# Performance work log

Hardware: AMD Instinct MI355X
Metric: run time of the kernel (lower is better)

The kernel has to match this reference:

```python
import jax, jax.numpy as jnp
import numpy as np

L = 3          # num_layers
EPS = 1e-5     # BatchNorm eps


def _gmn_forward(feats_1, feats_2, edge_index_1, edge_index_2, N1, N2,
                 Wn, bn, Wm, bm, Wp, bp, gamma, beta, Wa, ba, Wg, bg, Wf, bf):
    N = N1 + N2
    x = jnp.concatenate([feats_1, feats_2], axis=0)                       # [N, F]
    edge_index = jnp.concatenate([edge_index_1, edge_index_2 + N1], axis=1)
    src, dst = edge_index[0], edge_index[1]                               # source_to_target flow
    batch = jnp.concatenate([jnp.zeros((N1,), jnp.int32), jnp.ones((N2,), jnp.int32)])
    for l in range(L):
        h = x @ Wn[l] + bn[l]                                             # lin_node
        # message(x_i=h[dst], x_j=h[src]) = lin_message(cat[x_i, x_j])
        m = jnp.concatenate([h[dst], h[src]], axis=1) @ Wm[l] + bm[l]     # [E, D]
        aggr = jax.ops.segment_sum(m, dst, num_segments=N)                # scatter-add to targets
        # batch_block_pair_attention on ORIGINAL (pre-lin_node) features
        gx, gy = x[:N1], x[N1:]
        s = gx @ gy.T                                                     # [N1, N2] similarities
        att_x = jax.nn.softmax(s, axis=1) @ gy                            # attn for graph-1 nodes
        att_y = jax.nn.softmax(s, axis=0).T @ gx                          # attn for graph-2 nodes
        cross = jnp.concatenate([att_x, att_y], axis=0)                   # [N, F]
        att_in = x - cross                                                # attention_input
        out = jnp.concatenate([aggr, att_in], axis=1) @ Wp[l] + bp[l]     # lin_passing
        mu = out.mean(axis=0)
        var = ((out - mu) ** 2).mean(axis=0)                              # BatchNorm (train, biased var)
        x = (out - mu) * jax.lax.rsqrt(var + EPS) * gamma[l] + beta[l]
    # GraphAggregator
    states = x @ Wa + ba
    gates = jax.nn.softmax(x @ Wg + bg, axis=1)                           # softmax over feature dim (as in source)
    g = states * gates
    sums = jax.ops.segment_sum(g, batch, num_segments=2)                  # scatter_mean
    counts = jnp.array([N1, N2], jnp.float32)[:, None]
    emb = (sums / counts) @ Wf + bf                                       # [2, D]
    return emb


def setup_inputs() -> dict:
    key = jax.random.key(0)
    ks = jax.random.split(key, 12)
    N1 = N2 = 6144
    E = 196608
    F = 128
    D = 128
    sc = lambda fan: fan ** -0.5
    rn = lambda k, sh, s: jax.random.normal(k, sh, dtype=jnp.float32) * s
    return {
        "feats_1": rn(ks[0], (N1, F), 1.0),
        "edge_index_1": jax.random.randint(ks[1], (2, E), 0, N1),
        "feats_2": rn(ks[2], (N2, F), 1.0),
        "edge_index_2": jax.random.randint(ks[3], (2, E), 0, N2),
        "sizes_1": N1,
        "sizes_2": N2,
        "Wn": rn(ks[4], (L, F, D), sc(F)),
        "bn": jnp.zeros((L, D), jnp.float32),
        "Wm": rn(ks[5], (L, 2 * D, D), sc(2 * D)),
        "bm": jnp.zeros((L, D), jnp.float32),
        "Wp": rn(ks[6], (L, D + F, D), sc(D + F)),
        "bp": jnp.zeros((L, D), jnp.float32),
        "gamma": jnp.ones((L, D), jnp.float32),
        "beta": jnp.zeros((L, D), jnp.float32),
        "Wa": rn(ks[7], (D, D), sc(D)),
        "ba": jnp.zeros((D,), jnp.float32),
        "Wg": rn(ks[8], (D, D), sc(D)),
        "bg": jnp.zeros((D,), jnp.float32),
        "Wf": rn(ks[9], (D, D), sc(D)),
        "bf": jnp.zeros((D,), jnp.float32),
    }


def reference(feats_1, edge_index_1, feats_2, edge_index_2, sizes_1, sizes_2,
              Wn, bn, Wm, bm, Wp, bp, gamma, beta, Wa, ba, Wg, bg, Wf, bf):
    emb = _gmn_forward(feats_1, feats_2, edge_index_1, edge_index_2,
                       int(sizes_1), int(sizes_2),
                       Wn, bn, Wm, bm, Wp, bp, gamma, beta, Wa, ba, Wg, bg, Wf, bf)
    emb_1 = emb[0:1]
    emb_2 = emb[1:2]
    return emb_1, emb_2
```

## Files before the change

### kernel.cpp

```cpp
#include <hip/hip_runtime.h>
#include <hip/hip_bf16.h>

#define D 128
#define KVS 8
typedef unsigned short u16;
typedef unsigned int u32;
typedef __attribute__((ext_vector_type(8))) short short8;
typedef __attribute__((ext_vector_type(16))) float f32x16;
typedef __attribute__((ext_vector_type(4))) u32 u32x4;

__device__ __forceinline__ u16 f2bf(float f){
  u32 u = __builtin_bit_cast(u32, f);
  u32 r = (u + 0x7FFFu + ((u >> 16) & 1u)) >> 16;
  return (u16)r;
}
__device__ __forceinline__ float bf2f(u16 u){
  union { u32 i; float f; } v; v.i = ((u32)u) << 16; return v.f;
}

__global__ void k_copy(const float* __restrict__ src, float* __restrict__ dst, int n4){
  int i = blockIdx.x*blockDim.x + threadIdx.x;
  for (; i < n4; i += gridDim.x*blockDim.x){
    ((float4*)dst)[i] = ((const float4*)src)[i];
  }
}

__global__ void k_count(const int* __restrict__ ei1, const int* __restrict__ ei2,
                        int E1, int E2, int N1, int* __restrict__ cnt){
  int i = blockIdx.x*blockDim.x + threadIdx.x;
  int Et = E1 + E2;
  for (; i < Et; i += gridDim.x*blockDim.x){
    int dst = (i < E1) ? ei1[E1 + i] : (ei2[E2 + (i - E1)] + N1);
    atomicAdd(&cnt[dst], 1);
  }
}

__global__ void k_scan(const int* __restrict__ cnt, int* __restrict__ ptr,
                       int* __restrict__ cursor, float* __restrict__ degf, int N){
  __shared__ int part[256];
  int t = threadIdx.x;
  int per = (N + 255) >> 8;
  int lo = t*per, hi = min(N, lo+per);
  int s = 0;
  for (int j=lo;j<hi;j++) s += cnt[j];
  part[t] = s; __syncthreads();
  if (t==0){ int acc=0; for (int j=0;j<256;j++){ int v=part[j]; part[j]=acc; acc+=v; } }
  __syncthreads();
  int acc = part[t];
  for (int j=lo;j<hi;j++){ ptr[j]=acc; cursor[j]=acc; degf[j]=(float)cnt[j]; acc += cnt[j]; }
}

__global__ void k_fill(const int* __restrict__ ei1, const int* __restrict__ ei2,
                       int E1, int E2, int N1, int* __restrict__ cursor, int* __restrict__ srclist){
  int i = blockIdx.x*blockDim.x + threadIdx.x;
  int Et = E1 + E2;
  for (; i < Et; i += gridDim.x*blockDim.x){
    int src, dst;
    if (i < E1){ src = ei1[i]; dst = ei1[E1+i]; }
    else { int j = i - E1; src = ei2[j] + N1; dst = ei2[E2+j] + N1; }
    int p = atomicAdd(&cursor[dst], 1);
    srclist[p] = src;
  }
}

__global__ __launch_bounds__(256) void k_wcvt(const float* __restrict__ Wn, const float* __restrict__ Wm,
                                              const float* __restrict__ Wp, u16* __restrict__ wgt){
  __shared__ u16 tile[128][136];
  int m = blockIdx.x;
  const float* src; u16* dst;
  if (m < 3){ src = Wn + m*16384; dst = wgt + m*16384; }
  else if (m < 9){ int l=(m-3)%3, half=(m-3)/3; src = Wm + l*32768 + half*16384; dst = wgt + (3 + half*3 + l)*16384; }
  else { int l=(m-9)%3, half=(m-9)/3; src = Wp + l*32768 + half*16384; dst = wgt + (9 + half*3 + l)*16384; }
  int t = threadIdx.x;
  int n = t & 127, rh = t >> 7;
  for (int r0=0; r0<128; r0+=2){
    int r = r0 + rh;
    tile[n][r] = f2bf(src[r*128 + n]);
  }
  __syncthreads();
  int row = t >> 1, ch = t & 1;
  #pragma unroll
  for (int i=0;i<4;i++){
    int k0 = ch*64 + i*16;
    short8 a = *(const short8*)&tile[row][k0];
    short8 b = *(const short8*)&tile[row][k0+8];
    *(short8*)&dst[row*128 + k0] = a;
    *(short8*)&dst[row*128 + k0 + 8] = b;
  }
}

__global__ __launch_bounds__(256) void k_cvt(const float* __restrict__ x, u16* __restrict__ xb,
                                             u16* __restrict__ xbT, int N){
  __shared__ u16 tile[128][136];
  int nb = blockIdx.x * 128;
  int t = threadIdx.x;
  int n = t >> 1;
  int ch = t & 1;
  #pragma unroll
  for (int i=0;i<16;i++){
    int dd = ch*64 + i*4;
    float4 v = *(const float4*)&x[(size_t)(nb+n)*D + dd];
    u16 b0 = f2bf(v.x), b1 = f2bf(v.y), b2 = f2bf(v.z), b3 = f2bf(v.w);
    ushort4 uv; uv.x=b0; uv.y=b1; uv.z=b2; uv.w=b3;
    *(ushort4*)&xb[(size_t)(nb+n)*D + dd] = uv;
    tile[dd+0][n]=b0; tile[dd+1][n]=b1; tile[dd+2][n]=b2; tile[dd+3][n]=b3;
  }
  __syncthreads();
  int d = t & 127, hf = t >> 7;
  #pragma unroll
  for (int i=0;i<8;i++){
    short8 v = *(const short8*)&tile[d][hf*64 + i*8];
    *(short8*)&xbT[(size_t)d*N + nb + hf*64 + i*8] = v;
  }
}

__global__ __launch_bounds__(256) void k_gemm(
    const u16* __restrict__ A, const u16* __restrict__ W1T,
    const u16* __restrict__ B, const u16* __restrict__ W2T,
    const float* __restrict__ bias, const float* __restrict__ rs,
    const float* __restrict__ addin,
    float* __restrict__ of, u16* __restrict__ ob, int N)
{
  __shared__ __align__(16) u16 Wsw[2][16384];
  const int t = threadIdx.x;
  const int w4 = t >> 6;
  const int lane = t & 63;
  const int l31 = lane & 31;
  const int hi = lane >> 5;
  const int rb = blockIdx.x * 32;

  #pragma unroll
  for (int i=0;i<8;i++){
    int slot = i*256 + t;
    int row = slot >> 4, g = slot & 15;
    short8 v = *(const short8*)(W1T + row*128 + g*8);
    *(short8*)((char*)&Wsw[0][0] + row*256 + ((g ^ (row&7))*16)) = v;
  }
  if (B){
    #pragma unroll
    for (int i=0;i<8;i++){
      int slot = i*256 + t;
      int row = slot >> 4, g = slot & 15;
      short8 v = *(const short8*)(W2T + row*128 + g*8);
      *(short8*)((char*)&Wsw[1][0] + row*256 + ((g ^ (row&7))*16)) = v;
    }
  }
  short8 af[8], bfr[8];
  #pragma unroll
  for (int g=0; g<8; g++)
    af[g] = *(const short8*)(A + (size_t)(rb + l31)*D + (2*g + hi)*8);
  if (B){
    #pragma unroll
    for (int g=0; g<8; g++)
      bfr[g] = *(const short8*)(B + (size_t)(rb + l31)*D + (2*g + hi)*8);
  }
  __syncthreads();

  f32x16 acc1, acc2;
  #pragma unroll
  for (int i=0;i<16;i++){ acc1[i]=0.f; acc2[i]=0.f; }
  const int wrow = w4*32 + l31;
  #pragma unroll
  for (int s=0;s<8;s++){
    int gr = 2*s + hi;
    short8 wf = *(const short8*)((const char*)&Wsw[0][0] + wrow*256 + ((gr ^ (wrow&7))*16));
    acc1 = __builtin_amdgcn_mfma_f32_32x32x16_bf16(af[s], wf, acc1, 0,0,0);
  }
  if (B){
    #pragma unroll
    for (int s=0;s<8;s++){
      int gr = 2*s + hi;
      short8 wf = *(const short8*)((const char*)&Wsw[1][0] + wrow*256 + ((gr ^ (wrow&7))*16));
      acc2 = __builtin_amdgcn_mfma_f32_32x32x16_bf16(bfr[s], wf, acc2, 0,0,0);
    }
  }
  const int col = wrow;
  float bv = bias ? bias[col] : 0.0f;
  #pragma unroll
  for (int r=0;r<16;r++){
    int rr = (r&3) + 8*(r>>2) + 4*hi;
    size_t grow = (size_t)(rb + rr);
    float v = acc1[r] + bv;
    if (rs) v *= rs[grow];
    if (B) v += acc2[r];
    if (addin) v += addin[grow*D + col];
    if (of) of[grow*D + col] = v;
    if (ob) ob[grow*D + col] = f2bf(v);
  }
}

__global__ __launch_bounds__(256) void k_gather(const u16* __restrict__ hb, const int* __restrict__ ptr,
                          const int* __restrict__ cnt, const int* __restrict__ srclist,
                          float* __restrict__ Sg, int N){
  int f = threadIdx.x & 127, sub = threadIdx.x >> 7;
  int v = blockIdx.x*2 + sub;
  if (v >= N) return;
  int b = ptr[v], n = cnt[v];
  float a0=0.f, a1=0.f, a2=0.f, a3=0.f;
  int j=0;
  for (; j+3<n; j+=4){
    int s0=srclist[b+j], s1=srclist[b+j+1], s2=srclist[b+j+2], s3=srclist[b+j+3];
    a0 += bf2f(hb[(size_t)s0*D + f]);
    a1 += bf2f(hb[(size_t)s1*D + f]);
    a2 += bf2f(hb[(size_t)s2*D + f]);
    a3 += bf2f(hb[(size_t)s3*D + f]);
  }
  for (; j<n; j++) a0 += bf2f(hb[(size_t)srclist[b+j]*D + f]);
  Sg[(size_t)v*D + f] = (a0+a1)+(a2+a3);
}

__global__ __launch_bounds__(256, 2) void k_flash_mfma(
    const u16* __restrict__ xb, const u16* __restrict__ xbT,
    int N1, int N2, int Ntot,
    float* __restrict__ Opart, float* __restrict__ MLpart)
{
  __shared__ __align__(16) u16 Kbuf[2][4096];
  __shared__ __align__(16) u16 Vbuf[2][4096];

  const int t = threadIdx.x;
  const int w = t >> 6;
  const int lane = t & 63;
  const int l31 = lane & 31;
  const int hi = lane >> 5;

  const int qb = blockIdx.x / KVS;
  const int sp = blockIdx.x % KVS;
  const int qbase = qb * 128;
  const int qs = qbase + w*32;
  const bool isY = qbase >= N1;
  const int kv0 = isY ? 0 : N1;
  const int kvlen = isY ? N1 : N2;
  const int Lk = kvlen / KVS;
  const int kstart = kv0 + sp*Lk;
  const int ntiles = Lk >> 5;

  short8 qf[8];
  #pragma unroll
  for (int c = 0; c < 8; ++c)
    qf[c] = *(const short8*)(xb + (size_t)(qs + l31)*D + c*16 + hi*8);

  const int kr = t >> 3;
  const int kg = (t & 7) * 2;
  const int vd = t >> 1;
  const int vj = (t & 1) * 2;
  const int kw0 = kr*256 + ((kg     ^ (kr & 7))*16);
  const int kw1 = kr*256 + (((kg+1) ^ (kr & 7))*16);
  const int vw0 = vd*64  + (((vj     ^ vd) & 3)*16);
  const int vw1 = vd*64  + ((((vj+1) ^ vd) & 3)*16);

  f32x16 O[4];
  #pragma unroll
  for (int mt=0; mt<4; ++mt)
    #pragma unroll
    for (int i=0;i<16;i++) O[mt][i] = 0.f;
  float m_run = -3.0e38f, l_run = 0.0f;

  {
    int kb = kstart;
    short8 a0 = *(const short8*)(xb  + (size_t)(kb+kr)*D + kg*8);
    short8 a1 = *(const short8*)(xb  + (size_t)(kb+kr)*D + (kg+1)*8);
    short8 v0 = *(const short8*)(xbT + (size_t)vd*Ntot + kb + vj*8);
    short8 v1 = *(const short8*)(xbT + (size_t)vd*Ntot + kb + (vj+1)*8);
    *(short8*)((char*)&Kbuf[0][0] + kw0) = a0;
    *(short8*)((char*)&Kbuf[0][0] + kw1) = a1;
    *(short8*)((char*)&Vbuf[0][0] + vw0) = v0;
    *(short8*)((char*)&Vbuf[0][0] + vw1) = v1;
  }
  __syncthreads();

  for (int tt = 0; tt < ntiles; ++tt){
    const int cur = tt & 1;
    const int nxt = cur ^ 1;
    short8 a0, a1, v0, v1;
    const bool more = (tt+1 < ntiles);
    if (more){
      int kb = kstart + (tt+1)*32;
      a0 = *(const short8*)(xb  + (size_t)(kb+kr)*D + kg*8);
      a1 = *(const short8*)(xb  + (size_t)(kb+kr)*D + (kg+1)*8);
      v0 = *(const short8*)(xbT + (size_t)vd*Ntot + kb + vj*8);
      v1 = *(const short8*)(xbT + (size_t)vd*Ntot + kb + (vj+1)*8);
    }

    const char* Klds = (const char*)&Kbuf[cur][0];
    const char* Vlds = (const char*)&Vbuf[cur][0];

    f32x16 sa, sb;
    #pragma unroll
    for (int i=0;i<16;i++){ sa[i]=0.f; sb[i]=0.f; }
    #pragma unroll
    for (int c = 0; c < 8; c += 2){
      int gr0 = 2*c + hi;
      short8 ka = *(const short8*)(Klds + l31*256 + ((gr0 ^ (l31&7))*16));
      sa = __builtin_amdgcn_mfma_f32_32x32x16_bf16(ka, qf[c], sa, 0,0,0);
      int gr1 = 2*(c+1) + hi;
      short8 kbf = *(const short8*)(Klds + l31*256 + ((gr1 ^ (l31&7))*16));
      sb = __builtin_amdgcn_mfma_f32_32x32x16_bf16(kbf, qf[c+1], sb, 0,0,0);
    }
    f32x16 s;
    #pragma unroll
    for (int i=0;i<16;i++) s[i] = sa[i] + sb[i];

    float tm = s[0];
    #pragma unroll
    for (int i=1;i<16;i++) tm = fmaxf(tm, s[i]);
    tm = fmaxf(tm, __shfl_xor(tm, 32, 64));
    if (__any(tm > m_run + 8.0f)){
      float mnew = fmaxf(m_run, tm);
      float alpha = __expf(m_run - mnew);
      l_run *= alpha;
      m_run = mnew;
      #pragma unroll
      for (int i=0;i<16;i++){ O[0][i]*=alpha; O[1][i]*=alpha; O[2][i]*=alpha; O[3][i]*=alpha; }
    }
    float rsum = 0.f;
    #pragma unroll
    for (int i=0;i<16;i++){ float p = __expf(s[i]-m_run); s[i]=p; rsum += p; }
    rsum += __shfl_xor(rsum, 32, 64);
    l_run += rsum;

    u32 pk[8];
    #pragma unroll
    for (int i=0;i<8;i++){
      u32 r;
      asm("v_cvt_pk_bf16_f32 %0, %1, %2" : "=v"(r) : "v"(s[2*i]), "v"(s[2*i+1]));
      pk[i] = r;
    }

    #pragma unroll
    for (int ks=0; ks<2; ++ks){
      u32 send0 = hi ? pk[(2*ks)*2+0] : pk[(2*ks+1)*2+0];
      u32 send1 = hi ? pk[(2*ks)*2+1] : pk[(2*ks+1)*2+1];
      u32 xv0 = (u32)__shfl_xor((int)send0, 32, 64);
      u32 xv1 = (u32)__shfl_xor((int)send1, 32, 64);
      u32 own0 = hi ? pk[(2*ks+1)*2+0] : pk[(2*ks)*2+0];
      u32 own1 = hi ? pk[(2*ks+1)*2+1] : pk[(2*ks)*2+1];
      u32x4 bv;
      bv.x = hi ? xv0 : own0;
      bv.y = hi ? xv1 : own1;
      bv.z = hi ? own0 : xv0;
      bv.w = hi ? own1 : xv1;
      short8 pf = __builtin_bit_cast(short8, bv);
      #pragma unroll
      for (int mt=0; mt<4; ++mt){
        int dd = mt*32 + l31;
        int j = 2*ks + hi;
        short8 vf = *(const short8*)(Vlds + dd*64 + (((j ^ dd) & 3)*16));
        O[mt] = __builtin_amdgcn_mfma_f32_32x32x16_bf16(vf, pf, O[mt], 0,0,0);
      }
    }

    if (more){
      *(short8*)((char*)&Kbuf[nxt][0] + kw0) = a0;
      *(short8*)((char*)&Kbuf[nxt][0] + kw1) = a1;
      *(short8*)((char*)&Vbuf[nxt][0] + vw0) = v0;
      *(short8*)((char*)&Vbuf[nxt][0] + vw1) = v1;
    }
    __syncthreads();
  }

  const int strip = qs >> 5;
  float* Od = Opart + ((size_t)strip*KVS + sp)*4096;
  #pragma unroll
  for (int mt=0; mt<4; ++mt){
    #pragma unroll
    for (int r=0;r<16;r++){
      int dd = mt*32 + (r&3) + 8*(r>>2) + 4*hi;
      Od[dd*32 + l31] = O[mt][r];
    }
  }
  if (lane < 32){
    float* mlp = MLpart + ((size_t)strip*KVS + sp)*64;
    mlp[l31*2+0] = m_run;
    mlp[l31*2+1] = l_run;
  }
}

__global__ __launch_bounds__(256) void k_fcomb(
    const float* __restrict__ Opart, const float* __restrict__ MLpart,
    const float* __restrict__ x, u16* __restrict__ attinb)
{
  __shared__ float cw[KVS][32];
  __shared__ float Tld[128][33];
  const int strip = blockIdx.x;
  const int t = threadIdx.x;
  if (t < 32){
    int q = t;
    const float* mlp = MLpart + (size_t)strip*KVS*64;
    float mv[KVS], lv[KVS];
    float M = -3.0e38f;
    #pragma unroll
    for (int s2=0;s2<KVS;s2++){ mv[s2]=mlp[s2*64+q*2]; lv[s2]=mlp[s2*64+q*2+1]; M = fmaxf(M, mv[s2]); }
    float L = 0.f;
    #pragma unroll
    for (int s2=0;s2<KVS;s2++){ float wv=__expf(mv[s2]-M); cw[s2][q]=wv; L += wv*lv[s2]; }
    float inv = 1.0f / L;
    #pragma unroll
    for (int s2=0;s2<KVS;s2++) cw[s2][q] *= inv;
  }
  __syncthreads();
  {
    const int d = t >> 1, q0 = (t & 1) * 16;
    const float* Ob = Opart + (size_t)strip*KVS*4096;
    float acc[16];
    #pragma unroll
    for (int j=0;j<16;j++) acc[j]=0.f;
    #pragma unroll
    for (int s2=0; s2<KVS; ++s2){
      const float* row = Ob + s2*4096 + d*32 + q0;
      #pragma unroll
      for (int j4=0;j4<16;j4+=4){
        float4 v = *(const float4*)&row[j4];
        acc[j4+0] += cw[s2][q0+j4+0]*v.x;
        acc[j4+1] += cw[s2][q0+j4+1]*v.y;
        acc[j4+2] += cw[s2][q0+j4+2]*v.z;
        acc[j4+3] += cw[s2][q0+j4+3]*v.w;
      }
    }
    #pragma unroll
    for (int j=0;j<16;j++) Tld[d][q0+j] = acc[j];
  }
  __syncthreads();
  {
    const int q = t >> 3, c0 = (t & 7) * 16;
    const size_t row = (size_t)(strip*32 + q)*D;
    #pragma unroll
    for (int i=0;i<16;i+=4){
      float4 xr = *(const float4*)&x[row + c0 + i];
      ushort4 o;
      o.x = f2bf(xr.x - Tld[c0+i+0][q]);
      o.y = f2bf(xr.y - Tld[c0+i+1][q]);
      o.z = f2bf(xr.z - Tld[c0+i+2][q]);
      o.w = f2bf(xr.w - Tld[c0+i+3][q]);
      *(ushort4*)&attinb[row + c0 + i] = o;
    }
  }
}

__global__ __launch_bounds__(256) void k_colsum(const float* __restrict__ outb, int N,
                                                float* __restrict__ sums){
  int f = threadIdx.x & 127, sub = threadIdx.x >> 7;
  float s=0.f, q=0.f;
  for (int r = blockIdx.x*2 + sub; r < N; r += gridDim.x*2){
    float v = outb[(size_t)r*D + f]; s += v; q += v*v;
  }
  atomicAdd(&sums[f], s);
  atomicAdd(&sums[128+f], q);
}

__global__ __launch_bounds__(256) void k_normcvt(const float* __restrict__ outb,
                        const float* __restrict__ sums,
                        const float* __restrict__ gamma, const float* __restrict__ beta,
                        int N, float* __restrict__ x, u16* __restrict__ xb, u16* __restrict__ xbT){
  __shared__ u16 tile[128][136];
  __shared__ float smu[128], srs[128], sg2[128], sb2[128];
  int t = threadIdx.x;
  if (t < 128){
    float mu = sums[t] / (float)N;
    float var = fmaxf(sums[128+t]/(float)N - mu*mu, 0.0f);
    smu[t]=mu; srs[t]=rsqrtf(var + 1e-5f);
    sg2[t]=gamma[t]; sb2[t]=beta[t];
  }
  __syncthreads();
  int nb = blockIdx.x * 128;
  int n = t >> 1, ch = t & 1;
  #pragma unroll
  for (int i=0;i<16;i++){
    int dd = ch*64 + i*4;
    float4 v = *(const float4*)&outb[(size_t)(nb+n)*D + dd];
    float4 y;
    y.x = (v.x - smu[dd+0])*srs[dd+0]*sg2[dd+0] + sb2[dd+0];
    y.y = (v.y - smu[dd+1])*srs[dd+1]*sg2[dd+1] + sb2[dd+1];
    y.z = (v.z - smu[dd+2])*srs[dd+2]*sg2[dd+2] + sb2[dd+2];
    y.w = (v.w - smu[dd+3])*srs[dd+3]*sg2[dd+3] + sb2[dd+3];
    *(float4*)&x[(size_t)(nb+n)*D + dd] = y;
    u16 b0=f2bf(y.x), b1=f2bf(y.y), b2=f2bf(y.z), b3=f2bf(y.w);
    ushort4 uv; uv.x=b0; uv.y=b1; uv.z=b2; uv.w=b3;
    *(ushort4*)&xb[(size_t)(nb+n)*D + dd] = uv;
    tile[dd+0][n]=b0; tile[dd+1][n]=b1; tile[dd+2][n]=b2; tile[dd+3][n]=b3;
  }
  __syncthreads();
  int d = t & 127, hf = t >> 7;
  #pragma unroll
  for (int i=0;i<8;i++){
    short8 v = *(const short8*)&tile[d][hf*64 + i*8];
    *(short8*)&xbT[(size_t)d*N + nb + hf*64 + i*8] = v;
  }
}

__global__ __launch_bounds__(256) void k_matmul(
    const float* __restrict__ A, const float* __restrict__ W1,
    const float* __restrict__ bias, float* __restrict__ Y, int N)
{
  __shared__ float As[64][D];
  int t = threadIdx.x;
  int tx = t & 31, ty = t >> 5;
  int c0 = tx * 4;
  int rb = blockIdx.x * 64;
  if (rb >= N) return;
  for (int idx = t; idx < 64*32; idx += 256){
    int r = idx >> 5, cc = (idx & 31) * 4;
    *(float4*)&As[r][cc] = *(const float4*)&A[(size_t)(rb+r)*D + cc];
  }
  __syncthreads();
  float acc[8][4];
  #pragma unroll
  for (int i=0;i<8;i++){ acc[i][0]=0.f;acc[i][1]=0.f;acc[i][2]=0.f;acc[i][3]=0.f; }
  for (int k=0;k<D;k++){
    float4 wv = *(const float4*)&W1[k*D + c0];
    #pragma unroll
    for (int i=0;i<8;i++){
      float a = As[ty*8+i][k];
      acc[i][0] += a*wv.x; acc[i][1] += a*wv.y; acc[i][2] += a*wv.z; acc[i][3] += a*wv.w;
    }
  }
  float4 bv = *(const float4*)&bias[c0];
  #pragma unroll
  for (int i=0;i<8;i++){
    int r = rb + ty*8 + i;
    float4 o; o.x = acc[i][0] + bv.x; o.y = acc[i][1] + bv.y; o.z = acc[i][2] + bv.z; o.w = acc[i][3] + bv.w;
    *(float4*)&Y[(size_t)r*D + c0] = o;
  }
}

__global__ __launch_bounds__(256) void k_gatepool(
    const float* __restrict__ states, const float* __restrict__ glog,
    int N1, int N, float* __restrict__ gsums)
{
  __shared__ float part[256];
  part[threadIdx.x] = 0.f;
  __syncthreads();
  int wid = threadIdx.x >> 6, lane = threadIdx.x & 63;
  for (int v = blockIdx.x*4 + wid; v < N; v += gridDim.x*4){
    float a0 = glog[(size_t)v*D + lane], a1 = glog[(size_t)v*D + lane + 64];
    float mx = fmaxf(a0,a1);
    #pragma unroll
    for (int off=32; off; off>>=1) mx = fmaxf(mx, __shfl_xor(mx, off, 64));
    float e0 = __expf(a0-mx), e1 = __expf(a1-mx);
    float ss = e0+e1;
    #pragma unroll
    for (int off=32; off; off>>=1) ss += __shfl_xor(ss, off, 64);
    float inv = 1.f/ss;
    int g = (v < N1) ? 0 : 1;
    atomicAdd(&part[g*128 + lane], states[(size_t)v*D+lane]*e0*inv);
    atomicAdd(&part[g*128 + lane + 64], states[(size_t)v*D+lane+64]*e1*inv);
  }
  __syncthreads();
  atomicAdd(&gsums[threadIdx.x], part[threadIdx.x]);
}

__global__ __launch_bounds__(256) void k_emb(
    const float* __restrict__ gsums, const float* __restrict__ Wf,
    const float* __restrict__ bf_, int N1, int N2, float* __restrict__ outp)
{
  __shared__ float mean[256];
  int t = threadIdx.x;
  mean[t] = gsums[t] / ((t < 128) ? (float)N1 : (float)N2);
  __syncthreads();
  int g = t >> 7, dc = t & 127;
  float acc = bf_[dc];
  for (int k=0;k<D;k++) acc += mean[g*128 + k] * Wf[k*D + dc];
  outp[t] = acc;
}

extern "C" void kernel_launch(void* const* d_in, const int* in_sizes, int n_in,
                              void* d_out, int out_size, void* d_ws, size_t ws_size,
                              hipStream_t stream) {
  const float* feats1 = (const float*)d_in[0];
  const int*   ei1    = (const int*)d_in[1];
  const float* feats2 = (const float*)d_in[2];
  const int*   ei2    = (const int*)d_in[3];
  const float* Wn = (const float*)d_in[6];
  const float* bn = (const float*)d_in[7];
  const float* Wm = (const float*)d_in[8];
  const float* bm = (const float*)d_in[9];
  const float* Wp = (const float*)d_in[10];
  const float* bp = (const float*)d_in[11];
  const float* gamma = (const float*)d_in[12];
  const float* beta  = (const float*)d_in[13];
  const float* Wa = (const float*)d_in[14];
  const float* ba = (const float*)d_in[15];
  const float* Wg = (const float*)d_in[16];
  const float* bg = (const float*)d_in[17];
  const float* Wf = (const float*)d_in[18];
  const float* bff = (const float*)d_in[19];

  int N1 = in_sizes[0]/D, E1 = in_sizes[1]/2;
  int N2 = in_sizes[2]/D, E2 = in_sizes[3]/2;
  int N = N1+N2;
  int nstrips = N/32;

  char* w = (char*)d_ws;
  float* x    = (float*)w; w += (size_t)N*D*4;
  u16* xb     = (u16*)w;   w += (size_t)N*D*2;
  u16* xbT    = (u16*)w;   w += (size_t)N*D*2;
  u16* hb     = (u16*)w;   w += (size_t)N*D*2;
  u16* hm2b   = (u16*)w;   w += (size_t)N*D*2;
  u16* aggrb  = (u16*)w;   w += (size_t)N*D*2;
  u16* attinb = (u16*)w;   w += (size_t)N*D*2;
  int* cnt    = (int*)w;   w += (size_t)N*4;
  int* ptr    = (int*)w;   w += (size_t)N*4;
  int* cursor = (int*)w;   w += (size_t)N*4;
  float* degf = (float*)w; w += (size_t)N*4;
  int* srclist= (int*)w;   w += (size_t)(E1+E2)*4;
  float* sums = (float*)w; w += 1024;
  float* gsums= (float*)w; w += 1024;
  u16* wgt    = (u16*)w;   w += (size_t)15*16384*2;
  float* Opart = (float*)w; w += (size_t)nstrips*KVS*4096*4;
  float* MLpart= (float*)w; w += (size_t)nstrips*KVS*64*4;
  float* Sg     = Opart;
  float* outb   = Opart + (size_t)N*D;
  float* states = Opart;
  float* glog   = Opart + (size_t)N*D;

  hipMemsetAsync(cnt, 0, (size_t)N*4, stream);
  k_copy<<<768,256,0,stream>>>(feats1, x, N1*D/4);
  k_copy<<<768,256,0,stream>>>(feats2, x + (size_t)N1*D, N2*D/4);
  k_count<<<1024,256,0,stream>>>(ei1, ei2, E1, E2, N1, cnt);
  k_scan<<<1,256,0,stream>>>(cnt, ptr, cursor, degf, N);
  k_fill<<<1024,256,0,stream>>>(ei1, ei2, E1, E2, N1, cursor, srclist);
  k_wcvt<<<15,256,0,stream>>>(Wn, Wm, Wp, wgt);
  k_cvt<<<N/128,256,0,stream>>>(x, xb, xbT, N);

  for (int l=0;l<3;l++){
    const u16* WnT_l  = wgt + (size_t)(0+l)*16384;
    const u16* Wm1T_l = wgt + (size_t)(3+l)*16384;
    const u16* Wm2T_l = wgt + (size_t)(6+l)*16384;
    const u16* Wp1T_l = wgt + (size_t)(9+l)*16384;
    const u16* Wp2T_l = wgt + (size_t)(12+l)*16384;
    const float* bn_l = bn + (size_t)l*D;
    const float* bm_l = bm + (size_t)l*D;
    const float* bp_l = bp + (size_t)l*D;

    k_flash_mfma<<<(N/128)*KVS,256,0,stream>>>(xb, xbT, N1, N2, N, Opart, MLpart);
    k_fcomb<<<nstrips,256,0,stream>>>(Opart, MLpart, x, attinb);
    k_gemm<<<N/32,256,0,stream>>>(xb, WnT_l, nullptr, nullptr, bn_l, nullptr, nullptr, nullptr, hb, N);
    k_gemm<<<N/32,256,0,stream>>>(hb, Wm2T_l, nullptr, nullptr, nullptr, nullptr, nullptr, nullptr, hm2b, N);
    k_gather<<<N/2,256,0,stream>>>(hm2b, ptr, cnt, srclist, Sg, N);
    k_gemm<<<N/32,256,0,stream>>>(hb, Wm1T_l, nullptr, nullptr, bm_l, degf, Sg, nullptr, aggrb, N);
    k_gemm<<<N/32,256,0,stream>>>(aggrb, Wp1T_l, attinb, Wp2T_l, bp_l, nullptr, nullptr, outb, nullptr, N);
    hipMemsetAsync(sums, 0, 1024, stream);
    k_colsum<<<192,256,0,stream>>>(outb, N, sums);
    k_normcvt<<<N/128,256,0,stream>>>(outb, sums, gamma + (size_t)l*D, beta + (size_t)l*D, N, x, xb, xbT);
  }

  k_matmul<<<N/64,256,0,stream>>>(x, Wa, ba, states, N);
  k_matmul<<<N/64,256,0,stream>>>(x, Wg, bg, glog, N);
  hipMemsetAsync(gsums, 0, 1024, stream);
  k_gatepool<<<64,256,0,stream>>>(states, glog, N1, N, gsums);
  k_emb<<<1,256,0,stream>>>(gsums, Wf, bff, N1, N2, (float*)d_out);
}
```

Measured before the change: 719.3 us.

## Fold lin_node into message weights, fuse BN stats, bf16 flash partials, MFMA readout

Result: slower. 802.7 us (+11.6%).

```diff
diff --git a/kernel.cpp b/kernel.cpp
--- a/kernel.cpp
+++ b/kernel.cpp
@@ -16,13 +16,6 @@
 }
 __device__ __forceinline__ float bf2f(u16 u){
   union { u32 i; float f; } v; v.i = ((u32)u) << 16; return v.f;
-}
-
-__global__ void k_copy(const float* __restrict__ src, float* __restrict__ dst, int n4){
-  int i = blockIdx.x*blockDim.x + threadIdx.x;
-  for (; i < n4; i += gridDim.x*blockDim.x){
-    ((float4*)dst)[i] = ((const float4*)src)[i];
-  }
 }
 
 __global__ void k_count(const int* __restrict__ ei1, const int* __restrict__ ei2,
@@ -63,14 +56,14 @@
   }
 }
 
-__global__ __launch_bounds__(256) void k_wcvt(const float* __restrict__ Wn, const float* __restrict__ Wm,
-                                              const float* __restrict__ Wp, u16* __restrict__ wgt){
+__global__ __launch_bounds__(256) void k_wcvt(const float* __restrict__ Wp, const float* __restrict__ Wa,
+                                              const float* __restrict__ Wg, u16* __restrict__ wgt){
   __shared__ u16 tile[128][136];
   int m = blockIdx.x;
   const float* src; u16* dst;
-  if (m < 3){ src = Wn + m*16384; dst = wgt + m*16384; }
-  else if (m < 9){ int l=(m-3)%3, half=(m-3)/3; src = Wm + l*32768 + half*16384; dst = wgt + (3 + half*3 + l)*16384; }
-  else { int l=(m-9)%3, half=(m-9)/3; src = Wp + l*32768 + half*16384; dst = wgt + (9 + half*3 + l)*16384; }
+  if (m < 6){ int l = m % 3, half = m / 3; src = Wp + (size_t)l*32768 + half*16384; dst = wgt + (size_t)(half*3 + l)*16384; }
+  else if (m == 6){ src = Wa; dst = wgt + (size_t)6*16384; }
+  else { src = Wg; dst = wgt + (size_t)7*16384; }
   int t = threadIdx.x;
   int n = t & 127, rh = t >> 7;
   for (int r0=0; r0<128; r0+=2){
@@ -89,20 +82,60 @@
   }
 }
 
-__global__ __launch_bounds__(256) void k_cvt(const float* __restrict__ x, u16* __restrict__ xb,
-                                             u16* __restrict__ xbT, int N){
+__global__ __launch_bounds__(256) void k_wfuse(const float* __restrict__ Wn, const float* __restrict__ Wm,
+                                               const float* __restrict__ bn, const float* __restrict__ bm,
+                                               u16* __restrict__ wfu, float* __restrict__ fbias){
+  int blk = blockIdx.x;
+  int l = blk % 3, which = blk / 3;
+  const float* A  = Wn + (size_t)l*16384;
+  const float* Bm = Wm + (size_t)l*32768 + (which==0 ? 16384 : 0);
+  u16* dst  = wfu  + (size_t)(which==0 ? l : 3+l)*16384;
+  float* fb = fbias + (size_t)(which==0 ? l : 3+l)*128;
+  int t = threadIdx.x;
+  int c0 = (t & 31) * 4;
+  int r0 = (t >> 5) * 16;
+  float acc[16][4];
+  #pragma unroll
+  for (int i=0;i<16;i++){ acc[i][0]=0.f; acc[i][1]=0.f; acc[i][2]=0.f; acc[i][3]=0.f; }
+  for (int k=0;k<128;k++){
+    float4 b4 = *(const float4*)&Bm[k*128 + c0];
+    #pragma unroll
+    for (int i=0;i<16;i++){
+      float a = A[(r0+i)*128 + k];
+      acc[i][0] += a*b4.x; acc[i][1] += a*b4.y; acc[i][2] += a*b4.z; acc[i][3] += a*b4.w;
+    }
+  }
+  #pragma unroll
+  for (int i=0;i<16;i++)
+    #pragma unroll
+    for (int j=0;j<4;j++)
+      dst[(size_t)(c0+j)*128 + (r0+i)] = f2bf(acc[i][j]);
+  if (t < 128){
+    float s = 0.f;
+    for (int k=0;k<128;k++) s += bn[l*128+k]*Bm[k*128+t];
+    if (which) s += bm[l*128+t];
+    fb[t] = s;
+  }
+}
+
+__global__ __launch_bounds__(256) void k_cvt0(const float* __restrict__ src1, const float* __restrict__ src2,
+                                              int N1, float* __restrict__ x, u16* __restrict__ xb,
+                                              u16* __restrict__ xbT, int N){
   __shared__ u16 tile[128][136];
   int nb = blockIdx.x * 128;
   int t = threadIdx.x;
   int n = t >> 1;
   int ch = t & 1;
+  int row = nb + n;
+  const float* srow = (row < N1) ? &src1[(size_t)row*D] : &src2[(size_t)(row-N1)*D];
   #pragma unroll
   for (int i=0;i<16;i++){
     int dd = ch*64 + i*4;
-    float4 v = *(const float4*)&x[(size_t)(nb+n)*D + dd];
+    float4 v = *(const float4*)&srow[dd];
+    *(float4*)&x[(size_t)row*D + dd] = v;
     u16 b0 = f2bf(v.x), b1 = f2bf(v.y), b2 = f2bf(v.z), b3 = f2bf(v.w);
     ushort4 uv; uv.x=b0; uv.y=b1; uv.z=b2; uv.w=b3;
-    *(ushort4*)&xb[(size_t)(nb+n)*D + dd] = uv;
+    *(ushort4*)&xb[(size_t)row*D + dd] = uv;
     tile[dd+0][n]=b0; tile[dd+1][n]=b1; tile[dd+2][n]=b2; tile[dd+3][n]=b3;
   }
   __syncthreads();
@@ -119,7 +152,7 @@
     const u16* __restrict__ B, const u16* __restrict__ W2T,
     const float* __restrict__ bias, const float* __restrict__ rs,
     const float* __restrict__ addin,
-    float* __restrict__ of, u16* __restrict__ ob, int N)
+    float* __restrict__ of, u16* __restrict__ ob, float* __restrict__ csums, int N)
 {
   __shared__ __align__(16) u16 Wsw[2][16384];
   const int t = threadIdx.x;
@@ -176,6 +209,7 @@
   }
   const int col = wrow;
   float bv = bias ? bias[col] : 0.0f;
+  float ssum = 0.f, sq = 0.f;
   #pragma unroll
   for (int r=0;r<16;r++){
     int rr = (r&3) + 8*(r>>2) + 4*hi;
@@ -186,6 +220,11 @@
     if (addin) v += addin[grow*D + col];
     if (of) of[grow*D + col] = v;
     if (ob) ob[grow*D + col] = f2bf(v);
+    ssum += v; sq += v*v;
+  }
+  if (csums){
+    atomicAdd(&csums[col], ssum);
+    atomicAdd(&csums[128+col], sq);
   }
 }
 
@@ -212,11 +251,12 @@
 __global__ __launch_bounds__(256, 2) void k_flash_mfma(
     const u16* __restrict__ xb, const u16* __restrict__ xbT,
     int N1, int N2, int Ntot,
-    float* __restrict__ Opart, float* __restrict__ MLpart)
+    u16* __restrict__ Opartb, float* __restrict__ MLpart)
 {
   __shared__ __align__(16) u16 Kbuf[2][4096];
   __shared__ __align__(16) u16 Vbuf[2][4096];
 
+  const float L2E = 1.44269504f;
   const int t = threadIdx.x;
   const int w = t >> 6;
   const int lane = t & 63;
@@ -287,6 +327,7 @@
     f32x16 sa, sb;
     #pragma unroll
     for (int i=0;i<16;i++){ sa[i]=0.f; sb[i]=0.f; }
+    __builtin_amdgcn_s_setprio(1);
     #pragma unroll
     for (int c = 0; c < 8; c += 2){
       int gr0 = 2*c + hi;
@@ -296,6 +337,7 @@
       short8 kbf = *(const short8*)(Klds + l31*256 + ((gr1 ^ (l31&7))*16));
       sb = __builtin_amdgcn_mfma_f32_32x32x16_bf16(kbf, qf[c+1], sb, 0,0,0);
     }
+    __builtin_amdgcn_s_setprio(0);
     f32x16 s;
     #pragma unroll
     for (int i=0;i<16;i++) s[i] = sa[i] + sb[i];
@@ -304,9 +346,10 @@
     #pragma unroll
     for (int i=1;i<16;i++) tm = fmaxf(tm, s[i]);
     tm = fmaxf(tm, __shfl_xor(tm, 32, 64));
-    if (__any(tm > m_run + 8.0f)){
-      float mnew = fmaxf(m_run, tm);
-      float alpha = __expf(m_run - mnew);
+    float tm2 = tm * L2E;
+    if (__any(tm2 > m_run + 11.544f)){
+      float mnew = fmaxf(m_run, tm2);
+      float alpha = exp2f(m_run - mnew);
       l_run *= alpha;
       m_run = mnew;
       #pragma unroll
@@ -314,7 +357,7 @@
     }
     float rsum = 0.f;
     #pragma unroll
-    for (int i=0;i<16;i++){ float p = __expf(s[i]-m_run); s[i]=p; rsum += p; }
+    for (int i=0;i<16;i++){ float p = exp2f(fmaf(s[i], L2E, -m_run)); s[i]=p; rsum += p; }
     rsum += __shfl_xor(rsum, 32, 64);
     l_run += rsum;
 
@@ -340,6 +383,7 @@
       bv.z = hi ? own0 : xv0;
       bv.w = hi ? own1 : xv1;
       short8 pf = __builtin_bit_cast(short8, bv);
+      __builtin_amdgcn_s_setprio(1);
       #pragma unroll
       for (int mt=0; mt<4; ++mt){
         int dd = mt*32 + l31;
@@ -347,6 +391,7 @@
         short8 vf = *(const short8*)(Vlds + dd*64 + (((j ^ dd) & 3)*16));
         O[mt] = __builtin_amdgcn_mfma_f32_32x32x16_bf16(vf, pf, O[mt], 0,0,0);
       }
+      __builtin_amdgcn_s_setprio(0);
     }
 
     if (more){
@@ -359,13 +404,13 @@
   }
 
   const int strip = qs >> 5;
-  float* Od = Opart + ((size_t)strip*KVS + sp)*4096;
+  u16* Od = Opartb + ((size_t)strip*KVS + sp)*4096;
   #pragma unroll
   for (int mt=0; mt<4; ++mt){
     #pragma unroll
     for (int r=0;r<16;r++){
       int dd = mt*32 + (r&3) + 8*(r>>2) + 4*hi;
-      Od[dd*32 + l31] = O[mt][r];
+      Od[dd*32 + l31] = f2bf(O[mt][r]);
     }
   }
   if (lane < 32){
@@ -376,7 +421,7 @@
 }
 
 __global__ __launch_bounds__(256) void k_fcomb(
-    const float* __restrict__ Opart, const float* __restrict__ MLpart,
+    const u16* __restrict__ Opartb, const float* __restrict__ MLpart,
     const float* __restrict__ x, u16* __restrict__ attinb)
 {
   __shared__ float cw[KVS][32];
@@ -392,7 +437,7 @@
     for (int s2=0;s2<KVS;s2++){ mv[s2]=mlp[s2*64+q*2]; lv[s2]=mlp[s2*64+q*2+1]; M = fmaxf(M, mv[s2]); }
     float L = 0.f;
     #pragma unroll
-    for (int s2=0;s2<KVS;s2++){ float wv=__expf(mv[s2]-M); cw[s2][q]=wv; L += wv*lv[s2]; }
+    for (int s2=0;s2<KVS;s2++){ float wv=exp2f(mv[s2]-M); cw[s2][q]=wv; L += wv*lv[s2]; }
     float inv = 1.0f / L;
     #pragma unroll
     for (int s2=0;s2<KVS;s2++) cw[s2][q] *= inv;
@@ -400,20 +445,19 @@
   __syncthreads();
   {
     const int d = t >> 1, q0 = (t & 1) * 16;
-    const float* Ob = Opart + (size_t)strip*KVS*4096;
+    const u16* Ob = Opartb + (size_t)strip*KVS*4096;
     float acc[16];
     #pragma unroll
     for (int j=0;j<16;j++) acc[j]=0.f;
     #pragma unroll
     for (int s2=0; s2<KVS; ++s2){
-      const float* row = Ob + s2*4096 + d*32 + q0;
+      const u16* row = Ob + s2*4096 + d*32 + q0;
+      short8 v8a = *(const short8*)row;
+      short8 v8b = *(const short8*)(row + 8);
       #pragma unroll
-      for (int j4=0;j4<16;j4+=4){
-        float4 v = *(const float4*)&row[j4];
-        acc[j4+0] += cw[s2][q0+j4+0]*v.x;
-        acc[j4+1] += cw[s2][q0+j4+1]*v.y;
-        acc[j4+2] += cw[s2][q0+j4+2]*v.z;
-        acc[j4+3] += cw[s2][q0+j4+3]*v.w;
+      for (int j=0;j<8;j++){
+        acc[j]   += cw[s2][q0+j]  *bf2f((u16)v8a[j]);
+        acc[8+j] += cw[s2][q0+8+j]*bf2f((u16)v8b[j]);
       }
     }
     #pragma unroll
@@ -434,17 +478,6 @@
       *(ushort4*)&attinb[row + c0 + i] = o;
     }
   }
-}
-
-__global__ __launch_bounds__(256) void k_colsum(const float* __restrict__ outb, int N,
-                                                float* __restrict__ sums){
-  int f = threadIdx.x & 127, sub = threadIdx.x >> 7;
-  float s=0.f, q=0.f;
-  for (int r = blockIdx.x*2 + sub; r < N; r += gridDim.x*2){
-    float v = outb[(size_t)r*D + f]; s += v; q += v*v;
-  }
-  atomicAdd(&sums[f], s);
-  atomicAdd(&sums[128+f], q);
 }
 
 __global__ __launch_bounds__(256) void k_normcvt(const float* __restrict__ outb,
@@ -484,41 +517,6 @@
   for (int i=0;i<8;i++){
     short8 v = *(const short8*)&tile[d][hf*64 + i*8];
     *(short8*)&xbT[(size_t)d*N + nb + hf*64 + i*8] = v;
-  }
-}
-
-__global__ __launch_bounds__(256) void k_matmul(
-    const float* __restrict__ A, const float* __restrict__ W1,
-    const float* __restrict__ bias, float* __restrict__ Y, int N)
-{
-  __shared__ float As[64][D];
-  int t = threadIdx.x;
-  int tx = t & 31, ty = t >> 5;
-  int c0 = tx * 4;
-  int rb = blockIdx.x * 64;
-  if (rb >= N) return;
-  for (int idx = t; idx < 64*32; idx += 256){
-    int r = idx >> 5, cc = (idx & 31) * 4;
-    *(float4*)&As[r][cc] = *(const float4*)&A[(size_t)(rb+r)*D + cc];
-  }
-  __syncthreads();
-  float acc[8][4];
-  #pragma unroll
-  for (int i=0;i<8;i++){ acc[i][0]=0.f;acc[i][1]=0.f;acc[i][2]=0.f;acc[i][3]=0.f; }
-  for (int k=0;k<D;k++){
-    float4 wv = *(const float4*)&W1[k*D + c0];
-    #pragma unroll
-    for (int i=0;i<8;i++){
-      float a = As[ty*8+i][k];
-      acc[i][0] += a*wv.x; acc[i][1] += a*wv.y; acc[i][2] += a*wv.z; acc[i][3] += a*wv.w;
-    }
-  }
-  float4 bv = *(const float4*)&bias[c0];
-  #pragma unroll
-  for (int i=0;i<8;i++){
-    int r = rb + ty*8 + i;
-    float4 o; o.x = acc[i][0] + bv.x; o.y = acc[i][1] + bv.y; o.z = acc[i][2] + bv.z; o.w = acc[i][3] + bv.w;
-    *(float4*)&Y[(size_t)r*D + c0] = o;
   }
 }
 
@@ -593,7 +591,6 @@
   float* x    = (float*)w; w += (size_t)N*D*4;
   u16* xb     = (u16*)w;   w += (size_t)N*D*2;
   u16* xbT    = (u16*)w;   w += (size_t)N*D*2;
-  u16* hb     = (u16*)w;   w += (size_t)N*D*2;
   u16* hm2b   = (u16*)w;   w += (size_t)N*D*2;
   u16* aggrb  = (u16*)w;   w += (size_t)N*D*2;
   u16* attinb = (u16*)w;   w += (size_t)N*D*2;
@@ -604,47 +601,45 @@
   int* srclist= (int*)w;   w += (size_t)(E1+E2)*4;
   float* sums = (float*)w; w += 1024;
   float* gsums= (float*)w; w += 1024;
-  u16* wgt    = (u16*)w;   w += (size_t)15*16384*2;
-  float* Opart = (float*)w; w += (size_t)nstrips*KVS*4096*4;
-  float* MLpart= (float*)w; w += (size_t)nstrips*KVS*64*4;
-  float* Sg     = Opart;
-  float* outb   = Opart + (size_t)N*D;
-  float* states = Opart;
-  float* glog   = Opart + (size_t)N*D;
+  u16* wgt    = (u16*)w;   w += (size_t)8*16384*2;
+  u16* wfu    = (u16*)w;   w += (size_t)6*16384*2;
+  float* fbias= (float*)w; w += (size_t)6*128*4;
+  u16* Opartb = (u16*)w;   w += (size_t)nstrips*KVS*4096*2;
+  float* MLpart=(float*)w; w += (size_t)nstrips*KVS*64*4;
+  float* Sg     = (float*)Opartb;
+  float* outb   = (float*)Opartb + (size_t)N*D;
+  float* states = Sg;
+  float* glog   = outb;
 
   hipMemsetAsync(cnt, 0, (size_t)N*4, stream);
-  k_copy<<<768,256,0,stream>>>(feats1, x, N1*D/4);
-  k_copy<<<768,256,0,stream>>>(feats2, x + (size_t)N1*D, N2*D/4);
   k_count<<<1024,256,0,stream>>>(ei1, ei2, E1, E2, N1, cnt);
   k_scan<<<1,256,0,stream>>>(cnt, ptr, cursor, degf, N);
   k_fill<<<1024,256,0,stream>>>(ei1, ei2, E1, E2, N1, cursor, srclist);
-  k_wcvt<<<15,256,0,stream>>>(Wn, Wm, Wp, wgt);
-  k_cvt<<<N/128,256,0,stream>>>(x, xb, xbT, N);
+  k_wcvt<<<8,256,0,stream>>>(Wp, Wa, Wg, wgt);
+  k_wfuse<<<6,256,0,stream>>>(Wn, Wm, bn, bm, wfu, fbias);
+  k_cvt0<<<N/128,256,0,stream>>>(feats1, feats2, N1, x, xb, xbT, N);
 
   for (int l=0;l<3;l++){
-    const u16* WnT_l  = wgt + (size_t)(0+l)*16384;
-    const u16* Wm1T_l = wgt + (size_t)(3+l)*16384;
-    const u16* Wm2T_l = wgt + (size_t)(6+l)*16384;
-    const u16* Wp1T_l = wgt + (size_t)(9+l)*16384;
-    const u16* Wp2T_l = wgt + (size_t)(12+l)*16384;
-    const float* bn_l = bn + (size_t)l*D;
-    const float* bm_l = bm + (size_t)l*D;
+    const u16* fuse2T_l = wfu + (size_t)l*16384;
+    const u16* fuse1T_l = wfu + (size_t)(3+l)*16384;
+    const float* fb2_l  = fbias + (size_t)l*128;
+    const float* fb1_l  = fbias + (size_t)(3+l)*128;
+    const u16* Wp1T_l = wgt + (size_t)(0+l)*16384;
+    const u16* Wp2T_l = wgt + (size_t)(3+l)*16384;
     const float* bp_l = bp + (size_t)l*D;
 
-    k_flash_mfma<<<(N/128)*KVS,256,0,stream>>>(xb, xbT, N1, N2, N, Opart, MLpart);
-    k_fcomb<<<nstrips,256,0,stream>>>(Opart, MLpart, x, attinb);
-    k_gemm<<<N/32,256,0,stream>>>(xb, WnT_l, nullptr, nullptr, bn_l, nullptr, nullptr, nullptr, hb, N);
-    k_gemm<<<N/32,256,0,stream>>>(hb, Wm2T_l, nullptr, nullptr, nullptr, nullptr, nullptr, nullptr, hm2b, N);
+    k_flash_mfma<<<(N/128)*KVS,256,0,stream>>>(xb, xbT, N1, N2, N, Opartb, MLpart);
+    k_fcomb<<<nstrips,256,0,stream>>>(Opartb, MLpart, x, attinb);
+    k_gemm<<<N/32,256,0,stream>>>(xb, fuse2T_l, nullptr, nullptr, fb2_l, nullptr, nullptr, nullptr, hm2b, nullptr, N);
     k_gather<<<N/2,256,0,stream>>>(hm2b, ptr, cnt, srclist, Sg, N);
-    k_gemm<<<N/32,256,0,stream>>>(hb, Wm1T_l, nullptr, nullptr, bm_l, degf, Sg, nullptr, aggrb, N);
-    k_gemm<<<N/32,256,0,stream>>>(aggrb, Wp1T_l, attinb, Wp2T_l, bp_l, nullptr, nullptr, outb, nullptr, N);
+    k_gemm<<<N/32,256,0,stream>>>(xb, fuse1T_l, nullptr, nullptr, fb1_l, degf, Sg, nullptr, aggrb, nullptr, N);
     hipMemsetAsync(sums, 0, 1024, stream);
-    k_colsum<<<192,256,0,stream>>>(outb, N, sums);
+    k_gemm<<<N/32,256,0,stream>>>(aggrb, Wp1T_l, attinb, Wp2T_l, bp_l, nullptr, nullptr, outb, nullptr, sums, N);
     k_normcvt<<<N/128,256,0,stream>>>(outb, sums, gamma + (size_t)l*D, beta + (size_t)l*D, N, x, xb, xbT);
   }
 
-  k_matmul<<<N/64,256,0,stream>>>(x, Wa, ba, states, N);
-  k_matmul<<<N/64,256,0,stream>>>(x, Wg, bg, glog, N);
+  k_gemm<<<N/32,256,0,stream>>>(xb, wgt + (size_t)6*16384, nullptr, nullptr, ba, nullptr, nullptr, states, nullptr, nullptr, N);
+  k_gemm<<<N/32,256,0,stream>>>(xb, wgt + (size_t)7*16384, nullptr, nullptr, bg, nullptr, nullptr, glog, nullptr, nullptr, N);
   hipMemsetAsync(gsums, 0, 1024, stream);
   k_gatepool<<<64,256,0,stream>>>(states, glog, N1, N, gsums);
   k_emb<<<1,256,0,stream>>>(gsums, Wf, bff, N1, N2, (float*)d_out);
```
